# Kernel optimization log

Hardware: AMD Instinct MI355X
Metric: run time of the kernel (lower is better)

The kernel has to match this reference:

```python
import jax, jax.numpy as jnp
import numpy as np

H = 4  # head_num
K_CONV = 1  # convolution_num


def mhsa_mean(x, Wq, Wk, Wv, Wo):
    # x: [..., L, d]; standard multi-head self-attention followed by mean over L
    d = x.shape[-1]
    hd = d // H
    q = (x @ Wq).reshape(x.shape[:-1] + (H, hd))
    k = (x @ Wk).reshape(x.shape[:-1] + (H, hd))
    v = (x @ Wv).reshape(x.shape[:-1] + (H, hd))
    scores = jnp.einsum('...lhd,...mhd->...hlm', q, k) / jnp.sqrt(jnp.asarray(hd, x.dtype))
    attn = jax.nn.softmax(scores, axis=-1)
    o = jnp.einsum('...hlm,...mhd->...lhd', attn, v).reshape(x.shape) @ Wo
    return o.mean(axis=-2)


def setup_inputs() -> dict:
    key = jax.random.key(0)
    ks = jax.random.split(key, 18)
    WORD, QUERY, ENT, REV = 50000, 50000, 100000, 100000
    DW, DE = 64, 64
    LQ, LR, E, B = 8, 8, 2000000, 1024
    W_word = jax.random.normal(ks[0], (WORD, DW), jnp.float32) * 0.02
    W_word = W_word.at[0].set(0.0)  # padding_idx=0
    W_query = jax.random.normal(ks[1], (QUERY, DE), jnp.float32) * 0.02
    W_entity = jax.random.normal(ks[2], (ENT, DE), jnp.float32) * 0.02
    Wq = jax.random.normal(ks[3], (DW, DW), jnp.float32) * 0.05
    Wk = jax.random.normal(ks[4], (DW, DW), jnp.float32) * 0.05
    Wv = jax.random.normal(ks[5], (DW, DW), jnp.float32) * 0.05
    Wo = jax.random.normal(ks[6], (DW, DW), jnp.float32) * 0.05
    query_word_ids = jax.random.randint(ks[7], (QUERY, LQ), 0, WORD)
    review_word_ids = jax.random.randint(ks[8], (REV, LR), 0, WORD)
    profile_dst = jax.random.randint(ks[9], (REV,), 0, ENT)
    p_src = jax.random.randint(ks[10], (E,), 0, ENT)
    p_dst = jax.random.randint(ks[11], (E,), 0, ENT)
    p_qid = jax.random.randint(ks[12], (E,), 0, QUERY)
    users = jax.random.randint(ks[13], (B,), 0, ENT)
    items = jax.random.randint(ks[14], (B,), 0, ENT)
    negs = jax.random.randint(ks[15], (B,), 0, ENT)
    query_words = jax.random.randint(ks[16], (B, LQ), 0, WORD)
    return {'W_word': W_word, 'W_query': W_query, 'W_entity': W_entity,
            'Wq': Wq, 'Wk': Wk, 'Wv': Wv, 'Wo': Wo,
            'query_word_ids': query_word_ids, 'review_word_ids': review_word_ids,
            'profile_dst': profile_dst, 'p_src': p_src, 'p_dst': p_dst, 'p_qid': p_qid,
            'users': users, 'items': items, 'negs': negs, 'query_words': query_words}


def reference(W_word, W_query, W_entity, Wq, Wk, Wv, Wo,
              query_word_ids, review_word_ids, profile_dst, p_src, p_dst, p_qid,
              users, items, negs, query_words):
    N = W_entity.shape[0]
    DE = W_query.shape[1]
    # --- doc embeddings via MHSA+mean over composing words ---
    h_query = mhsa_mean(W_word[query_word_ids], Wq, Wk, Wv, Wo)    # [Q, DW]
    h_review = mhsa_mean(W_word[review_word_ids], Wq, Wk, Wv, Wo)  # [R, DW]
    # --- profiles: sum reviews into entities, degree-normalize ---
    deg_p = jnp.maximum(jax.ops.segment_sum(jnp.ones(profile_dst.shape[0], jnp.float32), profile_dst, num_segments=N), 1.0)
    ent_h = jax.ops.segment_sum(h_review, profile_dst, num_segments=N) / deg_p[:, None]
    q_e0 = jnp.concatenate([W_query, h_query], axis=-1)   # [Q, D]
    e_k = jnp.concatenate([W_entity, ent_h], axis=-1)     # e_0 [N, D]
    # --- interaction degrees: out-deg(purchased) + out-deg(purchased_by) ---
    ones_e = jnp.ones(p_src.shape[0], jnp.float32)
    deg_i = jax.ops.segment_sum(ones_e, p_src, num_segments=N) + jax.ops.segment_sum(ones_e, p_dst, num_segments=N)
    inv_sqrt = 1.0 / jnp.sqrt(jnp.maximum(deg_i, 1.0))    # [N]
    q_edge = q_e0[p_qid]                                   # [E, D]
    e_acc = e_k
    for _ in range(K_CONV):
        # purchased: m = src.e_k + q_e0[q_id] / sqrt(deg_i[src]); sum to dst
        msg = e_k[p_src] + q_edge * inv_sqrt[p_src][:, None]
        agg = jax.ops.segment_sum(msg, p_dst, num_segments=N)
        # purchased_by (reverse edges): m = e_k[src]/sqrt(deg_i[src]); sum to dst
        agg = agg + jax.ops.segment_sum(e_k[p_dst] * inv_sqrt[p_dst][:, None], p_src, num_segments=N)
        e_k = agg * inv_sqrt[:, None]
        e_acc = e_acc + e_k
    e = e_acc / (K_CONV + 1)                               # [N, D]
    # --- batch forward (train mode) ---
    qb = mhsa_mean(W_word[query_words], Wq, Wk, Wv, Wo)    # [B, DW]
    qb = jnp.concatenate([jnp.zeros((qb.shape[0], DE), qb.dtype), qb], axis=-1)
    personalized = e[users] + qb
    return personalized, e[items], e[negs]
```

## Files before the change

kernel.cpp:

```cpp
#include <hip/hip_runtime.h>

typedef unsigned int uint;
typedef unsigned short ushort;

typedef __bf16 bf16x8 __attribute__((ext_vector_type(8)));
typedef float f32x4 __attribute__((ext_vector_type(4)));
union U8 { uint4 u4; uint w[4]; bf16x8 b; };

__device__ __forceinline__ float bf2f(ushort u) {
    return __uint_as_float(((uint)u) << 16);
}
__device__ __forceinline__ float2 bfp2f(uint u) {
    float2 r;
    r.x = __uint_as_float(u << 16);
    r.y = __uint_as_float(u & 0xffff0000u);
    return r;
}
__device__ __forceinline__ ushort f2bf(float f) {
    uint u = __float_as_uint(f);
    return (ushort)((u + 0x7fffu + ((u >> 16) & 1u)) >> 16);
}
__device__ __forceinline__ uint4 pack8(float4 a, float4 b) {
    uint4 u;
    u.x = (uint)f2bf(a.x) | ((uint)f2bf(a.y) << 16);
    u.y = (uint)f2bf(a.z) | ((uint)f2bf(a.w) << 16);
    u.z = (uint)f2bf(b.x) | ((uint)f2bf(b.y) << 16);
    u.w = (uint)f2bf(b.z) | ((uint)f2bf(b.w) << 16);
    return u;
}

__global__ void mark_kernel(const int* __restrict__ users,
                            const int* __restrict__ items,
                            const int* __restrict__ negs,
                            int* __restrict__ mapid, int* __restrict__ mcnt,
                            int B) {
    int t = blockIdx.x * blockDim.x + threadIdx.x;
    if (t >= 3 * B) return;
    int n = t < B ? users[t] : (t < 2 * B ? items[t - B] : negs[t - 2 * B]);
    int old = atomicCAS(&mapid[n], -1, -2);
    if (old == -1) mapid[n] = atomicAdd(mcnt, 1);
}

__global__ void wswz_kernel(const float* __restrict__ Wq,
                            const float* __restrict__ Wk,
                            const float* __restrict__ Wv,
                            const float* __restrict__ Wo,
                            ushort* __restrict__ wsw, ushort* __restrict__ wswo) {
    int e = blockIdx.x * 256 + threadIdx.x;
    if (e < 12288) {
        int f = e >> 9, r = e & 511;
        int lane = r >> 3, i = r & 7;
        int ct = f >> 1, kh = f & 1;
        int k = kh * 32 + (lane >> 4) * 8 + i;
        int col = (ct & 3) * 16 + (lane & 15);
        const float* W = ct < 4 ? Wq : (ct < 8 ? Wk : Wv);
        wsw[f * 512 + lane * 8 + i] = f2bf(W[k * 64 + col]);
    } else if (e < 16384) {
        int e2 = e - 12288;
        int f = e2 >> 9, r = e2 & 511;
        int lane = r >> 3, i = r & 7;
        int ct = f >> 1, kh = f & 1;
        int k = kh * 32 + (lane >> 4) * 8 + i;
        int col = ct * 16 + (lane & 15);
        wswo[f * 512 + lane * 8 + i] = f2bf(Wo[k * 64 + col]);
    }
}

__global__ void pre_kernel(const float* __restrict__ W_word,
                           const ushort* __restrict__ wsw,
                           ushort* __restrict__ Pq, ushort* __restrict__ Pk,
                           ushort* __restrict__ Pv,
                           const float* __restrict__ W_query,
                           const float* __restrict__ W_entity,
                           ushort* __restrict__ qe0b, ushort* __restrict__ e0b,
                           const int* __restrict__ p_src,
                           const int* __restrict__ p_dst,
                           const int* __restrict__ profile_dst,
                           const int* __restrict__ mapid,
                           int* __restrict__ degc, int* __restrict__ degp,
                           int* __restrict__ deg2,
                           int WORD, int Qn, int N, int E, int R,
                           int nc_blk, int npj_blk, int ncq_blk, int nce_blk) {
    int bid = blockIdx.x;
    int g = bid >> 3, j = bid & 7;
    if ((g & 3) == 3) {
        int idx = (g >> 2) * 8 + j;
        if (idx >= nc_blk) return;
        int base = idx * 512 + threadIdx.x;
#pragma unroll
        for (int k = 0; k < 2; k++) {
            int t = base + k * 256;
            if (t < E) {
                int s = p_src[t], d = p_dst[t];
                atomicAdd(&degc[s], 1);
                atomicAdd(&degc[d], 1);
                int md = mapid[d]; if (md >= 0) atomicAdd(&deg2[md], 1);
                int ms = mapid[s]; if (ms >= 0) atomicAdd(&deg2[ms], 1);
            }
            if (t < R) atomicAdd(&degp[profile_dst[t]], 1);
        }
        return;
    }
    int idx = ((g >> 2) * 3 + (g & 3)) * 8 + j;
    if (idx < npj_blk) {
        int tile = idx * 4 + (threadIdx.x >> 6);
        if (tile * 16 >= WORD) return;
        int lane = threadIdx.x & 63, l15 = lane & 15, gi = lane >> 4;
        const float* xr = W_word + ((size_t)tile * 16 + l15) * 64 + gi * 8;
        U8 a0, a1;
        a0.u4 = pack8(*(const float4*)(xr), *(const float4*)(xr + 4));
        a1.u4 = pack8(*(const float4*)(xr + 32), *(const float4*)(xr + 36));
        const f32x4 zero4 = {0.f, 0.f, 0.f, 0.f};
#pragma unroll
        for (int ct = 0; ct < 12; ct++) {
            U8 b0, b1;
            b0.u4 = *(const uint4*)(wsw + (ct * 2 + 0) * 512 + lane * 8);
            b1.u4 = *(const uint4*)(wsw + (ct * 2 + 1) * 512 + lane * 8);
            f32x4 acc = __builtin_amdgcn_mfma_f32_16x16x32_bf16(a0.b, b0.b, zero4, 0, 0, 0);
            acc = __builtin_amdgcn_mfma_f32_16x16x32_bf16(a1.b, b1.b, acc, 0, 0, 0);
            ushort* dst = ct < 4 ? Pq : (ct < 8 ? Pk : Pv);
            int col = (ct & 3) * 16 + l15;
#pragma unroll
            for (int r = 0; r < 4; r++)
                dst[((size_t)tile * 16 + gi * 4 + r) * 64 + col] = f2bf(acc[r]);
        }
    } else if (idx < npj_blk + ncq_blk) {
        int t = (idx - npj_blk) * 256 + threadIdx.x;
        if (t >= Qn * 16) return;
        int r = t >> 4, c = (t & 15) * 4;
        const float4 v = *(const float4*)(W_query + (size_t)r * 64 + c);
        ushort4 o;
        o.x = f2bf(v.x); o.y = f2bf(v.y); o.z = f2bf(v.z); o.w = f2bf(v.w);
        *(ushort4*)(qe0b + (size_t)r * 128 + c) = o;
    } else if (idx < npj_blk + ncq_blk + nce_blk) {
        int t = (idx - npj_blk - ncq_blk) * 256 + threadIdx.x;
        if (t >= N * 16) return;
        int r = t >> 4, c = (t & 15) * 4;
        const float4 v = *(const float4*)(W_entity + (size_t)r * 64 + c);
        ushort4 o;
        o.x = f2bf(v.x); o.y = f2bf(v.y); o.z = f2bf(v.z); o.w = f2bf(v.w);
        *(ushort4*)(e0b + (size_t)r * 128 + c) = o;
    }
}

__global__ void scan_sum(const int* __restrict__ degp, int* __restrict__ csum,
                         int N) {
    __shared__ int red[4];
    int chunk = blockIdx.x, t = threadIdx.x;
    int base = chunk * 1024;
    int v = 0;
#pragma unroll
    for (int k = 0; k < 4; k++) {
        int idx = base + t * 4 + k;
        if (idx < N) v += degp[idx];
    }
#pragma unroll
    for (int o = 32; o; o >>= 1) v += __shfl_down(v, o, 64);
    if ((t & 63) == 0) red[t >> 6] = v;
    __syncthreads();
    if (t == 0) csum[chunk] = red[0] + red[1] + red[2] + red[3];
}

__global__ void scan_mid(int* __restrict__ csum, int nchunk,
                         const int* __restrict__ deg2,
                         int* __restrict__ offs2, int* __restrict__ cursor2,
                         int nb2) {
    __shared__ int lds[256];
    int t = threadIdx.x;
    int v = (t < nchunk) ? csum[t] : 0;
    lds[t] = v;
    __syncthreads();
    for (int o = 1; o < 256; o <<= 1) {
        int u = (t >= o) ? lds[t - o] : 0;
        __syncthreads();
        lds[t] += u;
        __syncthreads();
    }
    if (t < nchunk) csum[t] = lds[t] - v;
    __syncthreads();
    int k2 = nb2 >> 8;
    int s = 0;
    for (int k = 0; k < k2; k++) s += deg2[t * k2 + k];
    lds[t] = s;
    __syncthreads();
    for (int o = 1; o < 256; o <<= 1) {
        int u = (t >= o) ? lds[t - o] : 0;
        __syncthreads();
        lds[t] += u;
        __syncthreads();
    }
    int tb = lds[t] - s;
    for (int k = 0; k < k2; k++) {
        int dv = deg2[t * k2 + k];
        offs2[t * k2 + k] = tb;
        cursor2[t * k2 + k] = tb;
        tb += dv;
    }
    if (t == 255) offs2[nb2] = tb;
}

__global__ void scan_chunk(const int* __restrict__ degp,
                           const int* __restrict__ csum,
                           const int* __restrict__ degc,
                           int* __restrict__ offs_r, int* __restrict__ cursor_r,
                           float* __restrict__ inv, int N) {
    __shared__ int lds[256];
    int chunk = blockIdx.x, t = threadIdx.x;
    int base = chunk * 1024 + t * 4;
    int v0 = (base + 0 < N) ? degp[base + 0] : 0;
    int v1 = (base + 1 < N) ? degp[base + 1] : 0;
    int v2 = (base + 2 < N) ? degp[base + 2] : 0;
    int v3 = (base + 3 < N) ? degp[base + 3] : 0;
    if (base + 0 < N) inv[base + 0] = 1.0f / sqrtf((float)max(degc[base + 0], 1));
    if (base + 1 < N) inv[base + 1] = 1.0f / sqrtf((float)max(degc[base + 1], 1));
    if (base + 2 < N) inv[base + 2] = 1.0f / sqrtf((float)max(degc[base + 2], 1));
    if (base + 3 < N) inv[base + 3] = 1.0f / sqrtf((float)max(degc[base + 3], 1));
    int s = v0 + v1 + v2 + v3;
    lds[t] = s;
    __syncthreads();
    for (int o = 1; o < 256; o <<= 1) {
        int u = (t >= o) ? lds[t - o] : 0;
        __syncthreads();
        lds[t] += u;
        __syncthreads();
    }
    int tb = lds[t] - s + csum[chunk];
    int vv[4] = {v0, v1, v2, v3};
#pragma unroll
    for (int k = 0; k < 4; k++) {
        int idx = base + k;
        if (idx < N) {
            offs_r[idx] = tb; cursor_r[idx] = tb; tb += vv[k];
            if (idx == N - 1) offs_r[N] = tb;
        }
    }
}

__device__ __forceinline__ void mhsa_pair(const ushort* __restrict__ Pq,
                                          const ushort* __restrict__ Pk,
                                          const ushort* __restrict__ Pv,
                                          const int* __restrict__ ids,
                                          int wid2, int lane,
                                          ushort* __restrict__ outb) {
    const int l15 = lane & 15;
    const int gi  = lane >> 4;
    const int hs  = gi >> 1;
    const int dbase = (gi & 1) * 8;
    const int* idr = ids + (size_t)wid2 * 16;
    const bool valid = hs == (l15 >> 3);

    const int myid = idr[l15];
    int vid[8];
#pragma unroll
    for (int i = 0; i < 8; i++) vid[i] = idr[dbase + i];

    uint pk4[4][2];
    const f32x4 zero4 = {0.f, 0.f, 0.f, 0.f};
#pragma unroll
    for (int h = 0; h < 4; h++) {
        U8 a, b;
        if (valid) {
            a.u4 = *(const uint4*)(Pk + (size_t)myid * 64 + h * 16 + dbase);
            b.u4 = *(const uint4*)(Pq + (size_t)myid * 64 + h * 16 + dbase);
        } else {
            a.u4 = make_uint4(0, 0, 0, 0);
            b.u4 = make_uint4(0, 0, 0, 0);
        }
        f32x4 d = __builtin_amdgcn_mfma_f32_16x16x32_bf16(a.b, b.b, zero4, 0, 0, 0);
        float s0 = d[0] * 0.25f, s1 = d[1] * 0.25f;
        float s2 = d[2] * 0.25f, s3 = d[3] * 0.25f;
        if (!valid) { s0 = s1 = s2 = s3 = -1e30f; }
        float mx = fmaxf(fmaxf(s0, s1), fmaxf(s2, s3));
        mx = fmaxf(mx, __shfl_xor(mx, 16, 64));
        mx = fmaxf(mx, __shfl_xor(mx, 32, 64));
        float x0 = __expf(s0 - mx), x1 = __expf(s1 - mx);
        float x2 = __expf(s2 - mx), x3 = __expf(s3 - mx);
        float sm = x0 + x1 + x2 + x3;
        sm += __shfl_xor(sm, 16, 64);
        sm += __shfl_xor(sm, 32, 64);
        float f = 0.125f / sm;
        uint w0 = (uint)f2bf(x0 * f) | ((uint)f2bf(x1 * f) << 16);
        uint w1 = (uint)f2bf(x2 * f) | ((uint)f2bf(x3 * f) << 16);
        pk4[h][0] = valid ? w0 : 0u;
        pk4[h][1] = valid ? w1 : 0u;
    }

    const int srcA = l15 + (gi & 1) * 32;
    const int srcB = srcA + 16;
    const bool hi = gi >= 2;
    size_t vb[8];
#pragma unroll
    for (int i = 0; i < 8; i++) vb[i] = (size_t)vid[i] * 64;
#pragma unroll
    for (int t = 0; t < 4; t++) {
        uint aw0 = (uint)__shfl((int)pk4[t][0], srcA, 64);
        uint aw1 = (uint)__shfl((int)pk4[t][1], srcA, 64);
        uint aw2 = (uint)__shfl((int)pk4[t][0], srcB, 64);
        uint aw3 = (uint)__shfl((int)pk4[t][1], srcB, 64);
        U8 av_;
        av_.w[0] = hi ? 0u : aw0; av_.w[1] = hi ? 0u : aw1;
        av_.w[2] = hi ? 0u : aw2; av_.w[3] = hi ? 0u : aw3;
        uint e[8];
#pragma unroll
        for (int i = 0; i < 8; i++)
            e[i] = hi ? 0u : (uint)Pv[vb[i] + t * 16 + l15];
        U8 bv;
        bv.w[0] = e[0] | (e[1] << 16);
        bv.w[1] = e[2] | (e[3] << 16);
        bv.w[2] = e[4] | (e[5] << 16);
        bv.w[3] = e[6] | (e[7] << 16);
        f32x4 acc = __builtin_amdgcn_mfma_f32_16x16x32_bf16(av_.b, bv.b, zero4, 0, 0, 0);
        float s = acc[0] + acc[1] + acc[2] + acc[3];
        s += __shfl_xor(s, 16, 64);
        if ((gi & 1) == 0) {
            int row = wid2 * 2 + hs;
            outb[(size_t)row * 64 + t * 16 + l15] = f2bf(s);
        }
    }
}

__global__ void mega_kernel(const ushort* __restrict__ Pq,
                            const ushort* __restrict__ Pk,
                            const ushort* __restrict__ Pv,
                            const int* __restrict__ query_word_ids,
                            const int* __restrict__ review_word_ids,
                            const int* __restrict__ query_words,
                            ushort* __restrict__ hqom,
                            ushort* __restrict__ hrev,
                            ushort* __restrict__ omb,
                            const int* __restrict__ p_src,
                            const int* __restrict__ p_dst,
                            const int* __restrict__ p_qid,
                            const int* __restrict__ profile_dst,
                            const int* __restrict__ mapid,
                            int* __restrict__ cursor2, int2* __restrict__ list2,
                            int* __restrict__ cursor_r, int* __restrict__ rmsg,
                            int Qn, int R, int B, int E,
                            int nr_blk, int nq_blk, int nb_blk,
                            int np_blk, int nv_blk) {
    int bid = blockIdx.x;
    int g = bid >> 3, j = bid & 7;
    if ((g & 3) == 3) {
        int idx = (g >> 2) * 8 + j;
        if (idx < np_blk) {
            int base = idx * 512 + threadIdx.x;
#pragma unroll
            for (int k = 0; k < 2; k++) {
                int e = base + k * 256;
                if (e < E) {
                    int s = p_src[e], d = p_dst[e];
                    int md = mapid[d], ms = mapid[s];
                    if (md >= 0)
                        list2[atomicAdd(&cursor2[md], 1)] = make_int2(s, p_qid[e]);
                    if (ms >= 0)
                        list2[atomicAdd(&cursor2[ms], 1)] = make_int2(d, -1);
                }
            }
        } else if (idx < np_blk + nv_blk) {
            int r = (idx - np_blk) * 256 + threadIdx.x;
            if (r >= R) return;
            rmsg[atomicAdd(&cursor_r[profile_dst[r]], 1)] = r;
        }
        return;
    }
    int idx = ((g >> 2) * 3 + (g & 3)) * 8 + j;
    int lane = threadIdx.x & 63;
    int w = threadIdx.x >> 6;
    if (idx < nr_blk) {
        int wid2 = idx * 4 + w;
        if (wid2 < (R >> 1))
            mhsa_pair(Pq, Pk, Pv, review_word_ids, wid2, lane, hrev);
    } else if (idx < nr_blk + nq_blk) {
        int wid2 = (idx - nr_blk) * 4 + w;
        if (wid2 < (Qn >> 1))
            mhsa_pair(Pq, Pk, Pv, query_word_ids, wid2, lane, hqom);
    } else if (idx < nr_blk + nq_blk + nb_blk) {
        int wid2 = (idx - nr_blk - nq_blk) * 4 + w;
        if (wid2 < (B >> 1))
            mhsa_pair(Pq, Pk, Pv, query_words, wid2, lane, omb);
    }
}

__global__ void entity_gather(const ushort* __restrict__ hrev,
                              const int* __restrict__ offs_r,
                              const int* __restrict__ rmsg,
                              ushort* __restrict__ eom, int N) {
    int g = (blockIdx.x * blockDim.x + threadIdx.x) >> 4;
    int c = (threadIdx.x & 15) * 4;
    if (g >= N) return;
    int beg = offs_r[g], end = offs_r[g + 1];
    float a0 = 0.f, a1 = 0.f, a2 = 0.f, a3 = 0.f;
    for (int m = beg; m < end; m++) {
        int r = rmsg[m];
        ushort4 v = *(const ushort4*)(hrev + (size_t)r * 64 + c);
        a0 += bf2f(v.x); a1 += bf2f(v.y); a2 += bf2f(v.z); a3 += bf2f(v.w);
    }
    float s = 1.0f / (float)max(end - beg, 1);
    ushort4 o;
    o.x = f2bf(a0 * s); o.y = f2bf(a1 * s); o.z = f2bf(a2 * s); o.w = f2bf(a3 * s);
    *(ushort4*)(eom + (size_t)g * 64 + c) = o;
}

__global__ void wo_kernel(const ushort* __restrict__ eom,
                          const ushort* __restrict__ hqom,
                          const ushort* __restrict__ omb,
                          const ushort* __restrict__ wswo,
                          ushort* __restrict__ e0b, ushort* __restrict__ qe0b,
                          float* __restrict__ qb, int N, int Qn, int B) {
    int tile = blockIdx.x * 4 + (threadIdx.x >> 6);
    int ntile = (N + Qn + B) >> 4;
    if (tile >= ntile) return;
    int lane = threadIdx.x & 63, l15 = lane & 15, gi = lane >> 4;
    int row0 = tile << 4;
    int region; int rb;
    const ushort* src;
    if (row0 < N)            { region = 0; rb = row0;            src = eom; }
    else if (row0 < N + Qn)  { region = 1; rb = row0 - N;        src = hqom; }
    else                     { region = 2; rb = row0 - N - Qn;   src = omb; }
    const ushort* sr = src + ((size_t)rb + l15) * 64;
    U8 a0, a1;
    a0.u4 = *(const uint4*)(sr + gi * 8);
    a1.u4 = *(const uint4*)(sr + 32 + gi * 8);
    const f32x4 zero4 = {0.f, 0.f, 0.f, 0.f};
#pragma unroll
    for (int ct = 0; ct < 4; ct++) {
        U8 b0, b1;
        b0.u4 = *(const uint4*)(wswo + (ct * 2 + 0) * 512 + lane * 8);
        b1.u4 = *(const uint4*)(wswo + (ct * 2 + 1) * 512 + lane * 8);
        f32x4 acc = __builtin_amdgcn_mfma_f32_16x16x32_bf16(a0.b, b0.b, zero4, 0, 0, 0);
        acc = __builtin_amdgcn_mfma_f32_16x16x32_bf16(a1.b, b1.b, acc, 0, 0, 0);
        int col = ct * 16 + l15;
#pragma unroll
        for (int r = 0; r < 4; r++) {
            int row = rb + gi * 4 + r;
            if (region == 0)      e0b[(size_t)row * 128 + 64 + col] = f2bf(acc[r]);
            else if (region == 1) qe0b[(size_t)row * 128 + 64 + col] = f2bf(acc[r]);
            else                  qb[(size_t)row * 64 + col] = acc[r];
        }
    }
}

__global__ void gather_out(const ushort* __restrict__ e0b,
                           const ushort* __restrict__ qe0b,
                           const float* __restrict__ inv,
                           const int* __restrict__ mapid,
                           const int* __restrict__ offs2,
                           const int2* __restrict__ list2,
                           const float* __restrict__ qb,
                           const int* __restrict__ users,
                           const int* __restrict__ items,
                           const int* __restrict__ negs,
                           float* __restrict__ out, int B) {
    int slot = (blockIdx.x * blockDim.x + threadIdx.x) >> 4;
    int c = (threadIdx.x & 15) * 8;
    if (slot >= 3 * B) return;
    int which = slot / B, b = slot - which * B;
    int node = which == 0 ? users[b] : (which == 1 ? items[b] : negs[b]);
    int m = mapid[node];
    int beg = offs2[m], end = offs2[m + 1];
    float a0 = 0.f, a1 = 0.f, a2 = 0.f, a3 = 0.f;
    float a4 = 0.f, a5 = 0.f, a6 = 0.f, a7 = 0.f;
    for (int i = beg; i < end; i++) {
        int2 mm = list2[i];
        float w = inv[mm.x];
        const uint4 ev = *(const uint4*)(e0b + (size_t)mm.x * 128 + c);
        if (mm.y >= 0) {
            const uint4 qv = *(const uint4*)(qe0b + (size_t)mm.y * 128 + c);
            float2 e, q;
            e = bfp2f(ev.x); q = bfp2f(qv.x); a0 += fmaf(q.x, w, e.x); a1 += fmaf(q.y, w, e.y);
            e = bfp2f(ev.y); q = bfp2f(qv.y); a2 += fmaf(q.x, w, e.x); a3 += fmaf(q.y, w, e.y);
            e = bfp2f(ev.z); q = bfp2f(qv.z); a4 += fmaf(q.x, w, e.x); a5 += fmaf(q.y, w, e.y);
            e = bfp2f(ev.w); q = bfp2f(qv.w); a6 += fmaf(q.x, w, e.x); a7 += fmaf(q.y, w, e.y);
        } else {
            float2 e;
            e = bfp2f(ev.x); a0 = fmaf(e.x, w, a0); a1 = fmaf(e.y, w, a1);
            e = bfp2f(ev.y); a2 = fmaf(e.x, w, a2); a3 = fmaf(e.y, w, a3);
            e = bfp2f(ev.z); a4 = fmaf(e.x, w, a4); a5 = fmaf(e.y, w, a5);
            e = bfp2f(ev.w); a6 = fmaf(e.x, w, a6); a7 = fmaf(e.y, w, a7);
        }
    }
    float wn = inv[node];
    const uint4 sv = *(const uint4*)(e0b + (size_t)node * 128 + c);
    float2 e0v;
    float r0, r1, r2, r3, r4, r5, r6, r7;
    e0v = bfp2f(sv.x); r0 = 0.5f * fmaf(a0, wn, e0v.x); r1 = 0.5f * fmaf(a1, wn, e0v.y);
    e0v = bfp2f(sv.y); r2 = 0.5f * fmaf(a2, wn, e0v.x); r3 = 0.5f * fmaf(a3, wn, e0v.y);
    e0v = bfp2f(sv.z); r4 = 0.5f * fmaf(a4, wn, e0v.x); r5 = 0.5f * fmaf(a5, wn, e0v.y);
    e0v = bfp2f(sv.w); r6 = 0.5f * fmaf(a6, wn, e0v.x); r7 = 0.5f * fmaf(a7, wn, e0v.y);
    if (which == 0 && c >= 64) {
        const float4 q0 = *(const float4*)(qb + (size_t)b * 64 + (c - 64));
        const float4 q1 = *(const float4*)(qb + (size_t)b * 64 + (c - 60));
        r0 += q0.x; r1 += q0.y; r2 += q0.z; r3 += q0.w;
        r4 += q1.x; r5 += q1.y; r6 += q1.z; r7 += q1.w;
    }
    float* dst = out + (size_t)which * B * 128 + (size_t)b * 128 + c;
    float4 w0; w0.x = r0; w0.y = r1; w0.z = r2; w0.w = r3;
    float4 w1; w1.x = r4; w1.y = r5; w1.z = r6; w1.w = r7;
    *(float4*)dst = w0;
    *(float4*)(dst + 4) = w1;
}

extern "C" void kernel_launch(void* const* d_in, const int* in_sizes, int n_in,
                              void* d_out, int out_size, void* d_ws, size_t ws_size,
                              hipStream_t stream) {
    const float* W_word   = (const float*)d_in[0];
    const float* W_query  = (const float*)d_in[1];
    const float* W_entity = (const float*)d_in[2];
    const float* Wq       = (const float*)d_in[3];
    const float* Wk       = (const float*)d_in[4];
    const float* Wv       = (const float*)d_in[5];
    const float* Wo       = (const float*)d_in[6];
    const int* query_word_ids  = (const int*)d_in[7];
    const int* review_word_ids = (const int*)d_in[8];
    const int* profile_dst     = (const int*)d_in[9];
    const int* p_src  = (const int*)d_in[10];
    const int* p_dst  = (const int*)d_in[11];
    const int* p_qid  = (const int*)d_in[12];
    const int* users  = (const int*)d_in[13];
    const int* items  = (const int*)d_in[14];
    const int* negs   = (const int*)d_in[15];
    const int* query_words = (const int*)d_in[16];

    const int WORD = in_sizes[0] / 64;
    const int Qn   = in_sizes[1] / 64;
    const int N    = in_sizes[2] / 64;
    const int R    = in_sizes[8] / 8;
    const int E    = in_sizes[10];
    const int B    = in_sizes[13];

    const int NB2 = ((3 * B + 255) / 256) * 256;

    ushort* e0b  = (ushort*)d_ws;
    ushort* qe0b = e0b + (size_t)N * 128;
    ushort* Pq   = qe0b + (size_t)Qn * 128;
    ushort* Pk   = Pq + (size_t)WORD * 64;
    ushort* Pv   = Pk + (size_t)WORD * 64;
    ushort* hrev = Pv + (size_t)WORD * 64;
    ushort* hqom = hrev + (size_t)R * 64;
    ushort* omb  = hqom + (size_t)Qn * 64;
    ushort* eom  = omb + (size_t)B * 64;
    ushort* wsw  = eom + (size_t)N * 64;
    ushort* wswo = wsw + 12288;
    float*  qb   = (float*)(wswo + 4096);
    float*  inv  = qb + (size_t)B * 64;
    int* degc     = (int*)(inv + N);
    int* degp     = degc + N;
    int* deg2     = degp + N;
    int* mcnt     = deg2 + NB2;
    int* mapid    = mcnt + 4;
    int* offs_r   = mapid + N;
    int* cursor_r = offs_r + N + 2;
    int* csum     = cursor_r + N;
    int* offs2    = csum + 256;
    int* cursor2  = offs2 + NB2 + 2;
    int* rmsg     = cursor2 + NB2;
    int2* list2   = (int2*)(rmsg + R);

    const int nchunk = (N + 1023) / 1024;

    hipMemsetAsync(degc, 0, (2 * (size_t)N + NB2 + 4) * sizeof(int), stream);
    hipMemsetAsync(mapid, 0xFF, (size_t)N * sizeof(int), stream);

    mark_kernel<<<(3 * B + 255) / 256, 256, 0, stream>>>(users, items, negs,
                                                         mapid, mcnt, B);
    wswz_kernel<<<64, 256, 0, stream>>>(Wq, Wk, Wv, Wo, wsw, wswo);

    {
        int nc_blk  = (E + 511) / 512;
        int npj_blk = (WORD / 16 + 3) / 4;
        int ncq_blk = (Qn * 16 + 255) / 256;
        int nce_blk = (N * 16 + 255) / 256;
        int mh_fam  = npj_blk + ncq_blk + nce_blk;
        int T = max(4 * nc_blk, (mh_fam * 4 + 2) / 3);
        T = ((T + 31) / 32) * 32;
        pre_kernel<<<T, 256, 0, stream>>>(W_word, wsw, Pq, Pk, Pv,
                                          W_query, W_entity, qe0b, e0b,
                                          p_src, p_dst, profile_dst, mapid,
                                          degc, degp, deg2,
                                          WORD, Qn, N, E, R,
                                          nc_blk, npj_blk, ncq_blk, nce_blk);
    }

    scan_sum<<<nchunk, 256, 0, stream>>>(degp, csum, N);
    scan_mid<<<1, 256, 0, stream>>>(csum, nchunk, deg2, offs2, cursor2, NB2);
    scan_chunk<<<nchunk, 256, 0, stream>>>(degp, csum, degc, offs_r, cursor_r, inv, N);

    {
        int nr_blk = (R / 2 + 3) / 4;
        int nq_blk = (Qn / 2 + 3) / 4;
        int nb_blk = (B / 2 + 3) / 4;
        int np_blk = (E + 511) / 512;
        int nv_blk = (R + 255) / 256;
        int sc = np_blk + nv_blk;
        int mh = nr_blk + nq_blk + nb_blk;
        int T = max(4 * sc, (mh * 4 + 2) / 3);
        T = ((T + 31) / 32) * 32;
        mega_kernel<<<T, 256, 0, stream>>>(Pq, Pk, Pv,
                                           query_word_ids, review_word_ids, query_words,
                                           hqom, hrev, omb,
                                           p_src, p_dst, p_qid, profile_dst, mapid,
                                           cursor2, list2, cursor_r, rmsg,
                                           Qn, R, B, E,
                                           nr_blk, nq_blk, nb_blk, np_blk, nv_blk);
    }

    entity_gather<<<(N * 16 + 255) / 256, 256, 0, stream>>>(hrev, offs_r, rmsg, eom, N);

    {
        int ntile = (N + Qn + B) / 16;
        wo_kernel<<<(ntile + 3) / 4, 256, 0, stream>>>(eom, hqom, omb, wswo,
                                                       e0b, qe0b, qb, N, Qn, B);
    }

    gather_out<<<(3 * B * 16 + 255) / 256, 256, 0, stream>>>(e0b, qe0b, inv,
                                                             mapid, offs2, list2,
                                                             qb, users, items, negs,
                                                             (float*)d_out, B);
}
```

Baseline: 440.2 us.

## Compact relevant edges in pre pass and move degree counting into mega kernel

The first edge pass now builds a compacted list of edges that touch batch entities, using a wave-aggregated atomic to claim slots. The second pass then walks only that list instead of rescanning all 2M edges. The full degree histogram (degc) moves into mega_kernel, where it overlaps with the attention work, and a new small kernel computes the inverse square roots. This adds a kernel launch and an elist buffer placed after list2 at a fixed offset of 300000 entries, so list2 overflowing that bound would corrupt memory.

```diff
diff --git a/kernel.cpp b/kernel.cpp
--- a/kernel.cpp
+++ b/kernel.cpp
@@ -77,8 +77,8 @@
                            const int* __restrict__ p_dst,
                            const int* __restrict__ profile_dst,
                            const int* __restrict__ mapid,
-                           int* __restrict__ degc, int* __restrict__ degp,
-                           int* __restrict__ deg2,
+                           int* __restrict__ degp, int* __restrict__ deg2,
+                           uint* __restrict__ elist, int* __restrict__ ne,
                            int WORD, int Qn, int N, int E, int R,
                            int nc_blk, int npj_blk, int ncq_blk, int nce_blk) {
     int bid = blockIdx.x;
@@ -87,15 +87,28 @@
         int idx = (g >> 2) * 8 + j;
         if (idx >= nc_blk) return;
         int base = idx * 512 + threadIdx.x;
+        int lane = threadIdx.x & 63;
 #pragma unroll
         for (int k = 0; k < 2; k++) {
             int t = base + k * 256;
+            uint flags = 0;
             if (t < E) {
                 int s = p_src[t], d = p_dst[t];
-                atomicAdd(&degc[s], 1);
-                atomicAdd(&degc[d], 1);
-                int md = mapid[d]; if (md >= 0) atomicAdd(&deg2[md], 1);
-                int ms = mapid[s]; if (ms >= 0) atomicAdd(&deg2[ms], 1);
+                int md = mapid[d], ms = mapid[s];
+                if (md >= 0) { atomicAdd(&deg2[md], 1); flags |= 1u; }
+                if (ms >= 0) { atomicAdd(&deg2[ms], 1); flags |= 2u; }
+            }
+            unsigned long long mask = __ballot(flags != 0);
+            if (mask) {
+                int leader = __ffsll((long long)mask) - 1;
+                int cnt = __popcll(mask);
+                int pos = 0;
+                if (lane == leader) pos = atomicAdd(ne, cnt);
+                pos = __shfl(pos, leader, 64);
+                if (flags) {
+                    int pre = __popcll(mask & ((1ull << lane) - 1ull));
+                    elist[pos + pre] = (uint)t | (flags << 21);
+                }
             }
             if (t < R) atomicAdd(&degp[profile_dst[t]], 1);
         }
@@ -201,9 +214,8 @@
 
 __global__ void scan_chunk(const int* __restrict__ degp,
                            const int* __restrict__ csum,
-                           const int* __restrict__ degc,
                            int* __restrict__ offs_r, int* __restrict__ cursor_r,
-                           float* __restrict__ inv, int N) {
+                           int N) {
     __shared__ int lds[256];
     int chunk = blockIdx.x, t = threadIdx.x;
     int base = chunk * 1024 + t * 4;
@@ -211,10 +223,6 @@
     int v1 = (base + 1 < N) ? degp[base + 1] : 0;
     int v2 = (base + 2 < N) ? degp[base + 2] : 0;
     int v3 = (base + 3 < N) ? degp[base + 3] : 0;
-    if (base + 0 < N) inv[base + 0] = 1.0f / sqrtf((float)max(degc[base + 0], 1));
-    if (base + 1 < N) inv[base + 1] = 1.0f / sqrtf((float)max(degc[base + 1], 1));
-    if (base + 2 < N) inv[base + 2] = 1.0f / sqrtf((float)max(degc[base + 2], 1));
-    if (base + 3 < N) inv[base + 3] = 1.0f / sqrtf((float)max(degc[base + 3], 1));
     int s = v0 + v1 + v2 + v3;
     lds[t] = s;
     __syncthreads();
@@ -333,31 +341,47 @@
                             const int* __restrict__ p_qid,
                             const int* __restrict__ profile_dst,
                             const int* __restrict__ mapid,
+                            int* __restrict__ degc,
+                            const uint* __restrict__ elist,
+                            const int* __restrict__ ne,
                             int* __restrict__ cursor2, int2* __restrict__ list2,
                             int* __restrict__ cursor_r, int* __restrict__ rmsg,
                             int Qn, int R, int B, int E,
                             int nr_blk, int nq_blk, int nb_blk,
-                            int np_blk, int nv_blk) {
+                            int nd_blk, int npl_blk, int nv_blk) {
     int bid = blockIdx.x;
     int g = bid >> 3, j = bid & 7;
     if ((g & 3) == 3) {
         int idx = (g >> 2) * 8 + j;
-        if (idx < np_blk) {
-            int base = idx * 512 + threadIdx.x;
-#pragma unroll
-            for (int k = 0; k < 2; k++) {
-                int e = base + k * 256;
-                if (e < E) {
-                    int s = p_src[e], d = p_dst[e];
-                    int md = mapid[d], ms = mapid[s];
-                    if (md >= 0)
-                        list2[atomicAdd(&cursor2[md], 1)] = make_int2(s, p_qid[e]);
-                    if (ms >= 0)
-                        list2[atomicAdd(&cursor2[ms], 1)] = make_int2(d, -1);
+        if (idx < nd_blk) {
+            int base = idx * 1024 + threadIdx.x;
+#pragma unroll
+            for (int k = 0; k < 4; k++) {
+                int t = base + k * 256;
+                if (t < E) {
+                    atomicAdd(&degc[p_src[t]], 1);
+                    atomicAdd(&degc[p_dst[t]], 1);
                 }
             }
-        } else if (idx < np_blk + nv_blk) {
-            int r = (idx - np_blk) * 256 + threadIdx.x;
+        } else if (idx < nd_blk + npl_blk) {
+            int i0 = idx - nd_blk;
+            int nev = *ne;
+            for (int i = i0 * 256 + threadIdx.x; i < nev; i += npl_blk * 256) {
+                uint ent = elist[i];
+                int e = (int)(ent & 0x1FFFFFu);
+                uint flags = ent >> 21;
+                int s = p_src[e], d = p_dst[e];
+                if (flags & 1u) {
+                    int md = mapid[d];
+                    list2[atomicAdd(&cursor2[md], 1)] = make_int2(s, p_qid[e]);
+                }
+                if (flags & 2u) {
+                    int ms = mapid[s];
+                    list2[atomicAdd(&cursor2[ms], 1)] = make_int2(d, -1);
+                }
+            }
+        } else if (idx < nd_blk + npl_blk + nv_blk) {
+            int r = (idx - nd_blk - npl_blk) * 256 + threadIdx.x;
             if (r >= R) return;
             rmsg[atomicAdd(&cursor_r[profile_dst[r]], 1)] = r;
         }
@@ -379,6 +403,13 @@
         if (wid2 < (B >> 1))
             mhsa_pair(Pq, Pk, Pv, query_words, wid2, lane, omb);
     }
+}
+
+__global__ void inv_kernel(const int* __restrict__ degc,
+                           float* __restrict__ inv, int N) {
+    int t = blockIdx.x * blockDim.x + threadIdx.x;
+    if (t >= N) return;
+    inv[t] = 1.0f / sqrtf((float)max(degc[t], 1));
 }
 
 __global__ void entity_gather(const ushort* __restrict__ hrev,
@@ -547,7 +578,8 @@
     int* degp     = degc + N;
     int* deg2     = degp + N;
     int* mcnt     = deg2 + NB2;
-    int* mapid    = mcnt + 4;
+    int* ne       = mcnt + 4;
+    int* mapid    = ne + 4;
     int* offs_r   = mapid + N;
     int* cursor_r = offs_r + N + 2;
     int* csum     = cursor_r + N;
@@ -555,10 +587,11 @@
     int* cursor2  = offs2 + NB2 + 2;
     int* rmsg     = cursor2 + NB2;
     int2* list2   = (int2*)(rmsg + R);
+    uint* elist   = (uint*)(list2 + 300000);
 
     const int nchunk = (N + 1023) / 1024;
 
-    hipMemsetAsync(degc, 0, (2 * (size_t)N + NB2 + 4) * sizeof(int), stream);
+    hipMemsetAsync(degc, 0, (2 * (size_t)N + NB2 + 8) * sizeof(int), stream);
     hipMemsetAsync(mapid, 0xFF, (size_t)N * sizeof(int), stream);
 
     mark_kernel<<<(3 * B + 255) / 256, 256, 0, stream>>>(users, items, negs,
@@ -576,22 +609,23 @@
         pre_kernel<<<T, 256, 0, stream>>>(W_word, wsw, Pq, Pk, Pv,
                                           W_query, W_entity, qe0b, e0b,
                                           p_src, p_dst, profile_dst, mapid,
-                                          degc, degp, deg2,
+                                          degp, deg2, elist, ne,
                                           WORD, Qn, N, E, R,
                                           nc_blk, npj_blk, ncq_blk, nce_blk);
     }
 
     scan_sum<<<nchunk, 256, 0, stream>>>(degp, csum, N);
     scan_mid<<<1, 256, 0, stream>>>(csum, nchunk, deg2, offs2, cursor2, NB2);
-    scan_chunk<<<nchunk, 256, 0, stream>>>(degp, csum, degc, offs_r, cursor_r, inv, N);
+    scan_chunk<<<nchunk, 256, 0, stream>>>(degp, csum, offs_r, cursor_r, N);
 
     {
         int nr_blk = (R / 2 + 3) / 4;
         int nq_blk = (Qn / 2 + 3) / 4;
         int nb_blk = (B / 2 + 3) / 4;
-        int np_blk = (E + 511) / 512;
+        int nd_blk = (E + 1023) / 1024;
+        int npl_blk = 256;
         int nv_blk = (R + 255) / 256;
-        int sc = np_blk + nv_blk;
+        int sc = nd_blk + npl_blk + nv_blk;
         int mh = nr_blk + nq_blk + nb_blk;
         int T = max(4 * sc, (mh * 4 + 2) / 3);
         T = ((T + 31) / 32) * 32;
@@ -599,10 +633,14 @@
                                            query_word_ids, review_word_ids, query_words,
                                            hqom, hrev, omb,
                                            p_src, p_dst, p_qid, profile_dst, mapid,
+                                           degc, elist, ne,
                                            cursor2, list2, cursor_r, rmsg,
                                            Qn, R, B, E,
-                                           nr_blk, nq_blk, nb_blk, np_blk, nv_blk);
-    }
+                                           nr_blk, nq_blk, nb_blk,
+                                           nd_blk, npl_blk, nv_blk);
+    }
+
+    inv_kernel<<<(N + 255) / 256, 256, 0, stream>>>(degc, inv, N);
 
     entity_gather<<<(N * 16 + 255) / 256, 256, 0, stream>>>(hrev, offs_r, rmsg, eom, N);
 
```

Result: slower. 830.2 us (+88.6%).

## Move full-degree atomic counting from pre_kernel into mega_kernel scatter blocks

Applied to the files above, without the earlier changes.

Removes the degc atomic increments for every edge from pre_kernel and performs them in new block slots of mega_kernel, interleaved 1:1 with the MHSA blocks. The inverse-sqrt degree computation moves out of scan_chunk into a separate small inv_kernel launched after mega_kernel. The aim is to shorten the critical path through pre_kernel and the scans, and to overlap the atomic-heavy edge work with compute-bound attention work. It adds one kernel launch, and the mega_kernel grid now splits blocks evenly between the two families instead of 3:1.

```diff
diff --git a/kernel.cpp b/kernel.cpp
--- a/kernel.cpp
+++ b/kernel.cpp
@@ -77,8 +77,7 @@
                            const int* __restrict__ p_dst,
                            const int* __restrict__ profile_dst,
                            const int* __restrict__ mapid,
-                           int* __restrict__ degc, int* __restrict__ degp,
-                           int* __restrict__ deg2,
+                           int* __restrict__ degp, int* __restrict__ deg2,
                            int WORD, int Qn, int N, int E, int R,
                            int nc_blk, int npj_blk, int ncq_blk, int nce_blk) {
     int bid = blockIdx.x;
@@ -86,14 +85,12 @@
     if ((g & 3) == 3) {
         int idx = (g >> 2) * 8 + j;
         if (idx >= nc_blk) return;
-        int base = idx * 512 + threadIdx.x;
-#pragma unroll
-        for (int k = 0; k < 2; k++) {
+        int base = idx * 1024 + threadIdx.x;
+#pragma unroll
+        for (int k = 0; k < 4; k++) {
             int t = base + k * 256;
             if (t < E) {
                 int s = p_src[t], d = p_dst[t];
-                atomicAdd(&degc[s], 1);
-                atomicAdd(&degc[d], 1);
                 int md = mapid[d]; if (md >= 0) atomicAdd(&deg2[md], 1);
                 int ms = mapid[s]; if (ms >= 0) atomicAdd(&deg2[ms], 1);
             }
@@ -201,9 +198,8 @@
 
 __global__ void scan_chunk(const int* __restrict__ degp,
                            const int* __restrict__ csum,
-                           const int* __restrict__ degc,
                            int* __restrict__ offs_r, int* __restrict__ cursor_r,
-                           float* __restrict__ inv, int N) {
+                           int N) {
     __shared__ int lds[256];
     int chunk = blockIdx.x, t = threadIdx.x;
     int base = chunk * 1024 + t * 4;
@@ -211,10 +207,6 @@
     int v1 = (base + 1 < N) ? degp[base + 1] : 0;
     int v2 = (base + 2 < N) ? degp[base + 2] : 0;
     int v3 = (base + 3 < N) ? degp[base + 3] : 0;
-    if (base + 0 < N) inv[base + 0] = 1.0f / sqrtf((float)max(degc[base + 0], 1));
-    if (base + 1 < N) inv[base + 1] = 1.0f / sqrtf((float)max(degc[base + 1], 1));
-    if (base + 2 < N) inv[base + 2] = 1.0f / sqrtf((float)max(degc[base + 2], 1));
-    if (base + 3 < N) inv[base + 3] = 1.0f / sqrtf((float)max(degc[base + 3], 1));
     int s = v0 + v1 + v2 + v3;
     lds[t] = s;
     __syncthreads();
@@ -333,17 +325,28 @@
                             const int* __restrict__ p_qid,
                             const int* __restrict__ profile_dst,
                             const int* __restrict__ mapid,
+                            int* __restrict__ degc,
                             int* __restrict__ cursor2, int2* __restrict__ list2,
                             int* __restrict__ cursor_r, int* __restrict__ rmsg,
                             int Qn, int R, int B, int E,
                             int nr_blk, int nq_blk, int nb_blk,
-                            int np_blk, int nv_blk) {
+                            int nd_blk, int np_blk, int nv_blk) {
     int bid = blockIdx.x;
     int g = bid >> 3, j = bid & 7;
-    if ((g & 3) == 3) {
-        int idx = (g >> 2) * 8 + j;
-        if (idx < np_blk) {
-            int base = idx * 512 + threadIdx.x;
+    int idx = (g >> 1) * 8 + j;
+    if (g & 1) {
+        if (idx < nd_blk) {
+            int base = idx * 1024 + threadIdx.x;
+#pragma unroll
+            for (int k = 0; k < 4; k++) {
+                int t = base + k * 256;
+                if (t < E) {
+                    atomicAdd(&degc[p_src[t]], 1);
+                    atomicAdd(&degc[p_dst[t]], 1);
+                }
+            }
+        } else if (idx < nd_blk + np_blk) {
+            int base = (idx - nd_blk) * 512 + threadIdx.x;
 #pragma unroll
             for (int k = 0; k < 2; k++) {
                 int e = base + k * 256;
@@ -356,14 +359,13 @@
                         list2[atomicAdd(&cursor2[ms], 1)] = make_int2(d, -1);
                 }
             }
-        } else if (idx < np_blk + nv_blk) {
-            int r = (idx - np_blk) * 256 + threadIdx.x;
+        } else if (idx < nd_blk + np_blk + nv_blk) {
+            int r = (idx - nd_blk - np_blk) * 256 + threadIdx.x;
             if (r >= R) return;
             rmsg[atomicAdd(&cursor_r[profile_dst[r]], 1)] = r;
         }
         return;
     }
-    int idx = ((g >> 2) * 3 + (g & 3)) * 8 + j;
     int lane = threadIdx.x & 63;
     int w = threadIdx.x >> 6;
     if (idx < nr_blk) {
@@ -379,6 +381,13 @@
         if (wid2 < (B >> 1))
             mhsa_pair(Pq, Pk, Pv, query_words, wid2, lane, omb);
     }
+}
+
+__global__ void inv_kernel(const int* __restrict__ degc,
+                           float* __restrict__ inv, int N) {
+    int t = blockIdx.x * blockDim.x + threadIdx.x;
+    if (t >= N) return;
+    inv[t] = 1.0f / sqrtf((float)max(degc[t], 1));
 }
 
 __global__ void entity_gather(const ushort* __restrict__ hrev,
@@ -566,7 +575,7 @@
     wswz_kernel<<<64, 256, 0, stream>>>(Wq, Wk, Wv, Wo, wsw, wswo);
 
     {
-        int nc_blk  = (E + 511) / 512;
+        int nc_blk  = (E + 1023) / 1024;
         int npj_blk = (WORD / 16 + 3) / 4;
         int ncq_blk = (Qn * 16 + 255) / 256;
         int nce_blk = (N * 16 + 255) / 256;
@@ -576,33 +585,37 @@
         pre_kernel<<<T, 256, 0, stream>>>(W_word, wsw, Pq, Pk, Pv,
                                           W_query, W_entity, qe0b, e0b,
                                           p_src, p_dst, profile_dst, mapid,
-                                          degc, degp, deg2,
+                                          degp, deg2,
                                           WORD, Qn, N, E, R,
                                           nc_blk, npj_blk, ncq_blk, nce_blk);
     }
 
     scan_sum<<<nchunk, 256, 0, stream>>>(degp, csum, N);
     scan_mid<<<1, 256, 0, stream>>>(csum, nchunk, deg2, offs2, cursor2, NB2);
-    scan_chunk<<<nchunk, 256, 0, stream>>>(degp, csum, degc, offs_r, cursor_r, inv, N);
+    scan_chunk<<<nchunk, 256, 0, stream>>>(degp, csum, offs_r, cursor_r, N);
 
     {
         int nr_blk = (R / 2 + 3) / 4;
         int nq_blk = (Qn / 2 + 3) / 4;
         int nb_blk = (B / 2 + 3) / 4;
+        int nd_blk = (E + 1023) / 1024;
         int np_blk = (E + 511) / 512;
         int nv_blk = (R + 255) / 256;
-        int sc = np_blk + nv_blk;
+        int sc = nd_blk + np_blk + nv_blk;
         int mh = nr_blk + nq_blk + nb_blk;
-        int T = max(4 * sc, (mh * 4 + 2) / 3);
+        int T = 2 * max(sc, mh);
         T = ((T + 31) / 32) * 32;
         mega_kernel<<<T, 256, 0, stream>>>(Pq, Pk, Pv,
                                            query_word_ids, review_word_ids, query_words,
                                            hqom, hrev, omb,
                                            p_src, p_dst, p_qid, profile_dst, mapid,
-                                           cursor2, list2, cursor_r, rmsg,
+                                           degc, cursor2, list2, cursor_r, rmsg,
                                            Qn, R, B, E,
-                                           nr_blk, nq_blk, nb_blk, np_blk, nv_blk);
-    }
+                                           nr_blk, nq_blk, nb_blk,
+                                           nd_blk, np_blk, nv_blk);
+    }
+
+    inv_kernel<<<(N + 255) / 256, 256, 0, stream>>>(degc, inv, N);
 
     entity_gather<<<(N * 16 + 255) / 256, 256, 0, stream>>>(hrev, offs_r, rmsg, eom, N);
 
```

Result: slower. 504.0 us (+14.5%).
